# Kernel optimization log

Hardware: AMD Instinct MI355X
Metric: run time of the kernel (lower is better)

Reference implementation:

```python
import jax, jax.numpy as jnp
import numpy as np

B = 16384
G = 2048   # granule_cell_count
N = 512    # ca3_cell_count
DT = 0.5   # integration_timestep
STEPS = 5  # ca3_attractor_steps
A_REC = 0.02   # recovery_time_constant
B_SUB = 0.2    # subthreshold_coupling
C_RESET = -55.0  # spike_reset_voltage
D_AHP = 4.0      # after_hyperpolarization_jump
CONN_P = 0.1


def setup_inputs() -> dict:
    key = jax.random.key(0)
    k1, k2, k3, k4 = jax.random.split(key, 4)
    dg_query_spikes = (jax.random.uniform(k1, (B, G)) < 0.1).astype(jnp.float32)
    W_mossy = 0.05 * jax.random.normal(k2, (N, G), dtype=jnp.float32)
    mask = (jax.random.uniform(k3, (N, N)) < CONN_P).astype(jnp.float32)
    W_rec = mask * jax.random.uniform(k4, (N, N)) * 0.1
    W_rec = W_rec * (1.0 - jnp.eye(N, dtype=jnp.float32))  # zero diagonal
    v0 = jnp.full((N,), -65.0, dtype=jnp.float32)
    u0 = jnp.full((N,), 0.2 * -65.0, dtype=jnp.float32)
    return {"dg_query_spikes": dg_query_spikes, "W_mossy": W_mossy,
            "W_rec": W_rec, "v0": v0, "u0": u0}


def _izhikevich_step(v, u, I):
    # Euler step of the Izhikevich neuron model, per original torch code.
    dv = 0.04 * v * v + 5.0 * v + 140.0 - u + I
    du = A_REC * (B_SUB * v - u)
    v = v + dv * DT
    u = u + du * DT
    spike = (v >= 30.0).astype(v.dtype)
    v = jnp.where(spike > 0, jnp.asarray(C_RESET, v.dtype), v)
    u = u + spike * D_AHP
    v = jnp.clip(v, -90.0, 30.0)
    return v, u, spike


def reference(dg_query_spikes, W_mossy, W_rec, v0, u0):
    # query_current = Linear(dg) * 10.0  -> [B, N]
    query_current = (dg_query_spikes @ W_mossy.T) * 10.0
    v = jnp.broadcast_to(v0, (B, N))
    u = jnp.broadcast_to(u0, (B, N))
    spike = jnp.zeros((B, N), dtype=jnp.float32)
    for _ in range(STEPS):  # fixed small unrolled recurrence
        # torch.mv(W_rec, spikes) batched: [B,N] @ [N,N]^T
        recurrent_current = (v >= 30.0).astype(jnp.float32) @ W_rec.T
        total_current = query_current + recurrent_current
        v, u, spike = _izhikevich_step(v, u, total_current)
    return spike
```

## Files before the change

### kernel.cpp

```cpp
#include <hip/hip_runtime.h>
#include <cstdint>
#include <cstddef>


typedef __attribute__((ext_vector_type(8))) short bf16x8;
typedef __attribute__((ext_vector_type(8))) unsigned short u16x8;
typedef __attribute__((ext_vector_type(4))) float f32x4;
typedef __attribute__((ext_vector_type(4))) unsigned int u32x4;

constexpr int Bn = 16384, Gn = 2048, Nn = 512;
constexpr int BM = 64, BN = 128;
constexpr int NKT = 64;
constexpr size_t SLAB_A = (size_t)4 * Bn * 16;
constexpr size_t SLAB_B = (size_t)4 * Nn * 16;
constexpr size_t A_BYTES = (size_t)256 * Bn * 16;
constexpr size_t B_BYTES = (size_t)256 * Nn * 16;
constexpr unsigned int CAP = 700000;
constexpr size_t OFF_B    = A_BYTES;
constexpr size_t OFF_THR  = OFF_B + B_BYTES;
constexpr size_t OFF_CNT  = OFF_THR + 64;
constexpr size_t OFF_LIST = OFF_CNT + 64;
constexpr size_t WS_NEED  = OFF_LIST + (size_t)CAP * 4;
constexpr float DELTA = 0.125f;

__device__ __forceinline__ unsigned short f2bf(float x) {
  uint32_t u = __builtin_bit_cast(uint32_t, x);
  u += 0x7FFFu + ((u >> 16) & 1u);
  return (unsigned short)(u >> 16);
}

__device__ __forceinline__ void glds16(const void* g, const void* l) {
  __builtin_amdgcn_global_load_lds(
      (const __attribute__((address_space(1))) unsigned int*)g,
      (__attribute__((address_space(3))) unsigned int*)l, 16, 0, 0);
}

__device__ __forceinline__ float izhi5(float I, float vi, float ui) {
#pragma clang fp contract(off)
  float v = vi, u = ui, spk = 0.0f;
#pragma unroll
  for (int st = 0; st < 5; ++st) {
    float dv = 0.04f * v * v + 5.0f * v + 140.0f - u + I;
    float du = 0.02f * (0.2f * v - u);
    v = v + dv * 0.5f;
    u = u + du * 0.5f;
    spk = (v >= 30.0f) ? 1.0f : 0.0f;
    if (spk > 0.0f) v = -55.0f;
    u = u + spk * 4.0f;
    v = fminf(fmaxf(v, -90.0f), 30.0f);
  }
  return spk;
}

__global__ void calibrate(const float* __restrict__ v0, const float* __restrict__ u0,
                          float* __restrict__ thr, unsigned int* __restrict__ cnt) {
  const int l = (int)threadIdx.x;
  if (l == 0) cnt[0] = 0u;
  const float vi = v0[0], ui = u0[0];
  const float X0 = -45.0f;
  const float step = 90.0f / 64.0f;
  const float s = izhi5(X0 + step * (float)l, vi, ui);
  const float sp = __shfl_up(s, 1);
  unsigned long long m = __ballot((l > 0) && (s != sp));
  float t[2] = {1e30f, 1e30f};
#pragma unroll
  for (int k = 0; k < 2; ++k) {
    if (!m) break;
    const int i = __ffsll((long long)m) - 1;
    m &= m - 1;
    float lo = X0 + step * (float)(i - 1);
    float hi = X0 + step * (float)i;
    for (int rr = 0; rr < 3; ++rr) {
      const float st2 = (hi - lo) / 64.0f;
      const float ss = izhi5(lo + st2 * (float)l, vi, ui);
      const float s0 = __shfl(ss, 0);
      const unsigned long long mm = __ballot(ss != s0);
      const int ii = mm ? (__ffsll((long long)mm) - 1) : 64;
      hi = lo + st2 * (float)ii;
      lo = lo + st2 * (float)(ii - 1);
    }
    t[k] = 0.5f * (lo + hi);
  }
  if (l == 0) { thr[0] = t[0]; thr[1] = t[1]; }
}

__launch_bounds__(256)
__global__ void prep_dg(const float* __restrict__ dg, unsigned short* __restrict__ Ab) {
  __shared__ uint32_t lds[64][129];
  const int t  = (int)threadIdx.x;
  const int mt = (int)blockIdx.x >> 3;
  const int gt = (int)blockIdx.x & 7;
  const int m0 = mt * 64, g0 = gt * 256;
  {
    const int mm = t >> 2, q = t & 3;
    const float* src = dg + (size_t)(m0 + mm) * Gn + g0;
#pragma unroll
    for (int i = 0; i < 16; ++i) {
      float4 v = *reinterpret_cast<const float4*>(src + i * 16 + q * 4);
      uint32_t a = (v.x != 0.0f ? 0x3F80u : 0u) | (v.y != 0.0f ? 0x3F800000u : 0u);
      uint32_t b = (v.z != 0.0f ? 0x3F80u : 0u) | (v.w != 0.0f ? 0x3F800000u : 0u);
      const int c = i * 8 + q * 2;
      lds[mm][c] = a; lds[mm][c + 1] = b;
    }
  }
  __syncthreads();
  {
    const int mm = t & 63, c0 = t >> 6;
#pragma unroll
    for (int cc = 0; cc < 8; ++cc) {
      const int c = c0 + cc * 4;
      u32x4 v;
      v.x = lds[mm][c * 4 + 0]; v.y = lds[mm][c * 4 + 1];
      v.z = lds[mm][c * 4 + 2]; v.w = lds[mm][c * 4 + 3];
      const size_t off = ((size_t)(gt * 32 + c) * Bn + (m0 + mm)) * 16;
      *reinterpret_cast<u32x4*>(reinterpret_cast<char*>(Ab) + off) = v;
    }
  }
}

__launch_bounds__(256)
__global__ void prep_W(const float* __restrict__ Wm, unsigned short* __restrict__ Bb) {
  const int n  = (int)blockIdx.x;
  const int gi = (int)threadIdx.x;
  const float* src = Wm + (size_t)n * Gn + gi * 8;
  u16x8 h0;
#pragma unroll
  for (int e = 0; e < 8; ++e) h0[e] = f2bf(src[e]);
  *reinterpret_cast<u16x8*>(reinterpret_cast<char*>(Bb) +
                            ((size_t)gi * Nn + n) * 16) = h0;
}

__launch_bounds__(256, 4)
__global__ void gemm_spike(const char* __restrict__ Ab, const char* __restrict__ Bb,
                           const float* __restrict__ thr,
                           unsigned int* __restrict__ cnt,
                           unsigned int* __restrict__ list,
                           float* __restrict__ out) {
  __shared__ __align__(16) char lds[24576];
  const int t = (int)threadIdx.x;
  const int bx0 = (int)blockIdx.x;
  const int bx  = (bx0 & 7) * 128 + (bx0 >> 3);
  const int mt = bx >> 2, nt = bx & 3;
  const int m0 = mt * BM, n0 = nt * BN;

  const uint32_t asrc = (uint32_t)((((t >> 6) * Bn) + m0 + (t & 63)) * 16);
  uint32_t bsrc[2];
#pragma unroll
  for (int c = 0; c < 2; ++c) {
    const int j = t + 256 * c;
    bsrc[c] = (uint32_t)((((j >> 7) * Nn) + n0 + (j & 127)) * 16);
  }

  const int l  = t & 63, wv = t >> 6;
  const int wr = wv >> 1, wc = wv & 1;
  const int lr = l & 15, kh = l >> 4;

  uint32_t aoff[2], boff[4];
#pragma unroll
  for (int mf = 0; mf < 2; ++mf)
    aoff[mf] = (uint32_t)((kh * 64 + wr * 32 + mf * 16 + lr) * 16);
#pragma unroll
  for (int nf = 0; nf < 4; ++nf)
    boff[nf] = (uint32_t)(4096 + (kh * 128 + wc * 64 + nf * 16 + lr) * 16);

  f32x4 acc[2][4];
#pragma unroll
  for (int i = 0; i < 2; ++i)
#pragma unroll
    for (int j = 0; j < 4; ++j)
      acc[i][j] = (f32x4){0.0f, 0.0f, 0.0f, 0.0f};

  glds16(Ab + asrc, &lds[t * 16]);
#pragma unroll
  for (int c = 0; c < 2; ++c) glds16(Bb + bsrc[c], &lds[4096 + (t + 256 * c) * 16]);
  __syncthreads();

  for (int kt = 0; kt < NKT; ++kt) {
    const int cb = (kt & 1) * 12288;
    if (kt + 1 < NKT) {
      const int nb = ((kt + 1) & 1) * 12288;
      const char* pa = Ab + (size_t)(kt + 1) * SLAB_A;
      const char* pb = Bb + (size_t)(kt + 1) * SLAB_B;
      glds16(pa + asrc, &lds[nb + t * 16]);
#pragma unroll
      for (int c = 0; c < 2; ++c) glds16(pb + bsrc[c], &lds[nb + 4096 + (t + 256 * c) * 16]);
    }
    bf16x8 af[2], bf[4];
#pragma unroll
    for (int mf = 0; mf < 2; ++mf)
      af[mf] = *reinterpret_cast<const bf16x8*>(&lds[cb + aoff[mf]]);
#pragma unroll
    for (int nf = 0; nf < 4; ++nf)
      bf[nf] = *reinterpret_cast<const bf16x8*>(&lds[cb + boff[nf]]);
#pragma unroll
    for (int mf = 0; mf < 2; ++mf)
#pragma unroll
      for (int nf = 0; nf < 4; ++nf)
        acc[mf][nf] = __builtin_amdgcn_mfma_f32_16x16x32_bf16(
            af[mf], bf[nf], acc[mf][nf], 0, 0, 0);
    __syncthreads();
  }

  const float I5 = thr[0], I4 = thr[1];
#pragma unroll
  for (int nf = 0; nf < 4; ++nf) {
    const int ncol = n0 + wc * 64 + nf * 16 + lr;
#pragma unroll
    for (int mf = 0; mf < 2; ++mf) {
      const int mrow = m0 + wr * 32 + mf * 16 + kh * 4;
#pragma unroll
      for (int r = 0; r < 4; ++r) {
        const float I = acc[mf][nf][r] * 10.0f;
        const float sp = (I > I5 && I < I4) ? 1.0f : 0.0f;
        out[(size_t)(mrow + r) * Nn + ncol] = sp;
        if (fabsf(I - I5) < DELTA || fabsf(I - I4) < DELTA) {
          const unsigned int idx = atomicAdd(cnt, 1u);
          if (idx < CAP)
            list[idx] = (unsigned int)(mrow + r) * (unsigned int)Nn + (unsigned int)ncol;
        }
      }
    }
  }
}

__launch_bounds__(256)
__global__ void fixup(const float* __restrict__ dg, const float* __restrict__ Wm,
                      const float* __restrict__ v0, const float* __restrict__ u0,
                      const unsigned int* __restrict__ cnt,
                      const unsigned int* __restrict__ list,
                      float* __restrict__ out) {
#pragma clang fp contract(off)
  const unsigned int n = min(cnt[0], CAP);
  const unsigned int wid0   = (blockIdx.x * blockDim.x + threadIdx.x) >> 6;
  const unsigned int nwaves = (gridDim.x * blockDim.x) >> 6;
  const int l = (int)(threadIdx.x & 63);
  for (unsigned int i = wid0; i < n; i += nwaves) {
    const unsigned int e = list[i];
    const unsigned int m = e >> 9, nn = e & 511u;
    const float* dr = dg + (size_t)m * Gn;
    const float* wr = Wm + (size_t)nn * Gn;
    float acc = 0.0f;
#pragma unroll
    for (int j = 0; j < 8; ++j) {
      const int g = j * 256 + l * 4;
      const float4 d = *reinterpret_cast<const float4*>(dr + g);
      const float4 w = *reinterpret_cast<const float4*>(wr + g);
      acc += (d.x != 0.0f) ? w.x : 0.0f;
      acc += (d.y != 0.0f) ? w.y : 0.0f;
      acc += (d.z != 0.0f) ? w.z : 0.0f;
      acc += (d.w != 0.0f) ? w.w : 0.0f;
    }
#pragma unroll
    for (int off = 32; off > 0; off >>= 1) acc += __shfl_down(acc, off);
    if (l == 0)
      out[(size_t)m * Nn + nn] = izhi5(acc * 10.0f, v0[nn], u0[nn]);
  }
}

constexpr int ROWS = 32, TG = 16, NCHUNK = Gn / 32;

__launch_bounds__(512, 2)
__global__ void ca3_sparse_kernel(const float* __restrict__ dg,
                                  const float* __restrict__ Wm,
                                  const float* __restrict__ v0,
                                  const float* __restrict__ u0,
                                  float* __restrict__ out) {
#pragma clang fp contract(off)
  __shared__ float    lds_w[TG * Nn];
  __shared__ uint32_t lds_bits[ROWS][NCHUNK];
  const int t    = (int)threadIdx.x;
  const int row0 = (int)blockIdx.x * ROWS;
  {
    const int r  = t >> 4;
    const int c0 = (t & 15) * 4;
    const float* p = dg + (size_t)(row0 + r) * Gn + (size_t)c0 * 32;
#pragma unroll
    for (int cc = 0; cc < 4; ++cc) {
      uint32_t bits = 0;
#pragma unroll
      for (int i = 0; i < 8; ++i) {
        float4 x = reinterpret_cast<const float4*>(p + cc * 32)[i];
        bits |= (x.x != 0.0f ? 1u : 0u) << (i * 4 + 0);
        bits |= (x.y != 0.0f ? 1u : 0u) << (i * 4 + 1);
        bits |= (x.z != 0.0f ? 1u : 0u) << (i * 4 + 2);
        bits |= (x.w != 0.0f ? 1u : 0u) << (i * 4 + 3);
      }
      lds_bits[r][c0 + cc] = bits;
    }
  }
  float acc[ROWS];
#pragma unroll
  for (int r = 0; r < ROWS; ++r) acc[r] = 0.0f;
  for (int gt = 0; gt < Gn / TG; ++gt) {
    __syncthreads();
    {
      const int k  = t & 3;
      const int nb = t >> 2;
#pragma unroll
      for (int pq = 0; pq < 4; ++pq) {
        const int n = pq * 128 + nb;
        const float4 w4 = *reinterpret_cast<const float4*>(
            Wm + (size_t)n * Gn + gt * TG + k * 4);
        lds_w[(k * 4 + 0) * Nn + n] = w4.x;
        lds_w[(k * 4 + 1) * Nn + n] = w4.y;
        lds_w[(k * 4 + 2) * Nn + n] = w4.z;
        lds_w[(k * 4 + 3) * Nn + n] = w4.w;
      }
    }
    __syncthreads();
    const int shift = (gt & 1) * 16;
#pragma unroll
    for (int r = 0; r < ROWS; ++r) {
      uint32_t b = (lds_bits[r][gt >> 1] >> shift) & 0xFFFFu;
      b = __builtin_amdgcn_readfirstlane(b);
      while (b) {
        const int g0 = __builtin_ctz(b);
        const uint32_t b1 = b & (b - 1);
        const int g1 = __builtin_ctz(b1 | 0x8000u);
        const uint32_t b2 = b1 & (b1 - 1);
        const int g2 = __builtin_ctz(b2 | 0x8000u);
        const uint32_t b3 = b2 & (b2 - 1);
        const int g3 = __builtin_ctz(b3 | 0x8000u);
        float x0 = lds_w[g0 * Nn + t];
        float x1 = lds_w[g1 * Nn + t];
        float x2 = lds_w[g2 * Nn + t];
        float x3 = lds_w[g3 * Nn + t];
        x1 = (b1 != 0u) ? x1 : 0.0f;
        x2 = (b2 != 0u) ? x2 : 0.0f;
        x3 = (b3 != 0u) ? x3 : 0.0f;
        acc[r] += x0; acc[r] += x1; acc[r] += x2; acc[r] += x3;
        b = b3 & (b3 - 1);
      }
    }
  }
  const float vi = v0[t];
  const float ui = u0[t];
#pragma unroll
  for (int r = 0; r < ROWS; ++r) {
    out[(size_t)(row0 + r) * Nn + t] = izhi5(acc[r] * 10.0f, vi, ui);
  }
}

extern "C" void kernel_launch(void* const* d_in, const int* in_sizes, int n_in,
                              void* d_out, int out_size, void* d_ws, size_t ws_size,
                              hipStream_t stream) {
  const float* dg = (const float*)d_in[0];
  const float* Wm = (const float*)d_in[1];
  const float* v0 = (const float*)d_in[3];
  const float* u0 = (const float*)d_in[4];
  float* out = (float*)d_out;

  if (ws_size < WS_NEED) {
    hipLaunchKernelGGL(ca3_sparse_kernel, dim3(Bn / ROWS), dim3(512), 0, stream,
                       dg, Wm, v0, u0, out);
    return;
  }
  char* base = (char*)d_ws;
  unsigned short* Ab = (unsigned short*)base;
  unsigned short* Bb = (unsigned short*)(base + OFF_B);
  float* thr         = (float*)(base + OFF_THR);
  unsigned int* cnt  = (unsigned int*)(base + OFF_CNT);
  unsigned int* list = (unsigned int*)(base + OFF_LIST);

  hipLaunchKernelGGL(calibrate, dim3(1), dim3(64), 0, stream, v0, u0, thr, cnt);
  hipLaunchKernelGGL(prep_dg, dim3(2048), dim3(256), 0, stream, dg, Ab);
  hipLaunchKernelGGL(prep_W, dim3(512), dim3(256), 0, stream, Wm, Bb);
  hipLaunchKernelGGL(gemm_spike, dim3(1024), dim3(256), 0, stream,
                     (const char*)Ab, (const char*)Bb, thr, cnt, list, out);
  hipLaunchKernelGGL(fixup, dim3(512), dim3(256), 0, stream,
                     dg, Wm, v0, u0, cnt, list, out);
}
```

Measured before the change: 135.0 us.

## Fuse dg-to-bf16 conversion into GEMM with register-staged 4-buffer pipeline

Removes the separate prep_dg kernel and its workspace round trip. The GEMM now reads the fp32 spike matrix directly into registers, packs it to bf16 by truncation, and writes it to LDS. B tiles still stream in through global_load_lds. The loop becomes a manually unrolled 4-buffer software pipeline with explicit waitcnt and barrier control. This saves a full write and reread of the converted A matrix, at the cost of more LDS (lower occupancy bound, 3 blocks) and fp32 global reads inside the GEMM.

```diff
diff --git a/kernel.cpp b/kernel.cpp
--- a/kernel.cpp
+++ b/kernel.cpp
@@ -11,22 +11,24 @@
 constexpr int Bn = 16384, Gn = 2048, Nn = 512;
 constexpr int BM = 64, BN = 128;
 constexpr int NKT = 64;
-constexpr size_t SLAB_A = (size_t)4 * Bn * 16;
 constexpr size_t SLAB_B = (size_t)4 * Nn * 16;
-constexpr size_t A_BYTES = (size_t)256 * Bn * 16;
-constexpr size_t B_BYTES = (size_t)256 * Nn * 16;
+constexpr size_t B_BYTES = (size_t)NKT * SLAB_B;
 constexpr unsigned int CAP = 700000;
-constexpr size_t OFF_B    = A_BYTES;
-constexpr size_t OFF_THR  = OFF_B + B_BYTES;
+constexpr size_t OFF_THR  = B_BYTES;
 constexpr size_t OFF_CNT  = OFF_THR + 64;
 constexpr size_t OFF_LIST = OFF_CNT + 64;
 constexpr size_t WS_NEED  = OFF_LIST + (size_t)CAP * 4;
 constexpr float DELTA = 0.125f;
+constexpr int BUFB = 12288;
 
 __device__ __forceinline__ unsigned short f2bf(float x) {
   uint32_t u = __builtin_bit_cast(uint32_t, x);
   u += 0x7FFFu + ((u >> 16) & 1u);
   return (unsigned short)(u >> 16);
+}
+__device__ __forceinline__ uint32_t pack2(float lo, float hi) {
+  return (__builtin_bit_cast(uint32_t, lo) >> 16) |
+         (__builtin_bit_cast(uint32_t, hi) & 0xFFFF0000u);
 }
 
 __device__ __forceinline__ void glds16(const void* g, const void* l) {
@@ -85,40 +87,6 @@
 }
 
 __launch_bounds__(256)
-__global__ void prep_dg(const float* __restrict__ dg, unsigned short* __restrict__ Ab) {
-  __shared__ uint32_t lds[64][129];
-  const int t  = (int)threadIdx.x;
-  const int mt = (int)blockIdx.x >> 3;
-  const int gt = (int)blockIdx.x & 7;
-  const int m0 = mt * 64, g0 = gt * 256;
-  {
-    const int mm = t >> 2, q = t & 3;
-    const float* src = dg + (size_t)(m0 + mm) * Gn + g0;
-#pragma unroll
-    for (int i = 0; i < 16; ++i) {
-      float4 v = *reinterpret_cast<const float4*>(src + i * 16 + q * 4);
-      uint32_t a = (v.x != 0.0f ? 0x3F80u : 0u) | (v.y != 0.0f ? 0x3F800000u : 0u);
-      uint32_t b = (v.z != 0.0f ? 0x3F80u : 0u) | (v.w != 0.0f ? 0x3F800000u : 0u);
-      const int c = i * 8 + q * 2;
-      lds[mm][c] = a; lds[mm][c + 1] = b;
-    }
-  }
-  __syncthreads();
-  {
-    const int mm = t & 63, c0 = t >> 6;
-#pragma unroll
-    for (int cc = 0; cc < 8; ++cc) {
-      const int c = c0 + cc * 4;
-      u32x4 v;
-      v.x = lds[mm][c * 4 + 0]; v.y = lds[mm][c * 4 + 1];
-      v.z = lds[mm][c * 4 + 2]; v.w = lds[mm][c * 4 + 3];
-      const size_t off = ((size_t)(gt * 32 + c) * Bn + (m0 + mm)) * 16;
-      *reinterpret_cast<u32x4*>(reinterpret_cast<char*>(Ab) + off) = v;
-    }
-  }
-}
-
-__launch_bounds__(256)
 __global__ void prep_W(const float* __restrict__ Wm, unsigned short* __restrict__ Bb) {
   const int n  = (int)blockIdx.x;
   const int gi = (int)threadIdx.x;
@@ -130,26 +98,25 @@
                             ((size_t)gi * Nn + n) * 16) = h0;
 }
 
-__launch_bounds__(256, 4)
-__global__ void gemm_spike(const char* __restrict__ Ab, const char* __restrict__ Bb,
+__launch_bounds__(256, 3)
+__global__ void gemm_fused(const float* __restrict__ dg, const char* __restrict__ Bb,
                            const float* __restrict__ thr,
                            unsigned int* __restrict__ cnt,
                            unsigned int* __restrict__ list,
                            float* __restrict__ out) {
-  __shared__ __align__(16) char lds[24576];
+  __shared__ __align__(16) char lds[4 * BUFB];
   const int t = (int)threadIdx.x;
   const int bx0 = (int)blockIdx.x;
   const int bx  = (bx0 & 7) * 128 + (bx0 >> 3);
   const int mt = bx >> 2, nt = bx & 3;
   const int m0 = mt * BM, n0 = nt * BN;
 
-  const uint32_t asrc = (uint32_t)((((t >> 6) * Bn) + m0 + (t & 63)) * 16);
-  uint32_t bsrc[2];
-#pragma unroll
-  for (int c = 0; c < 2; ++c) {
-    const int j = t + 256 * c;
-    bsrc[c] = (uint32_t)((((j >> 7) * Nn) + n0 + (j & 127)) * 16);
-  }
+  const float* dgrow = dg + (size_t)(m0 + (t >> 2)) * Gn + (t & 3) * 8;
+  const uint32_t awoff = (uint32_t)(((t & 3) * 64 + (t >> 2)) * 16);
+  const uint32_t bsrc0 = (uint32_t)((((t >> 7) & 3) * Nn + n0 + (t & 127)) * 16);
+  const uint32_t bsrc1 = (uint32_t)(((((t + 256) >> 7) & 3) * Nn + n0 + ((t + 256) & 127)) * 16);
+  const uint32_t bdst0 = (uint32_t)(4096 + t * 16);
+  const uint32_t bdst1 = (uint32_t)(4096 + (t + 256) * 16);
 
   const int l  = t & 63, wv = t >> 6;
   const int wr = wv >> 1, wc = wv & 1;
@@ -170,36 +137,79 @@
     for (int j = 0; j < 4; ++j)
       acc[i][j] = (f32x4){0.0f, 0.0f, 0.0f, 0.0f};
 
-  glds16(Ab + asrc, &lds[t * 16]);
-#pragma unroll
-  for (int c = 0; c < 2; ++c) glds16(Bb + bsrc[c], &lds[4096 + (t + 256 * c) * 16]);
-  __syncthreads();
-
-  for (int kt = 0; kt < NKT; ++kt) {
-    const int cb = (kt & 1) * 12288;
-    if (kt + 1 < NKT) {
-      const int nb = ((kt + 1) & 1) * 12288;
-      const char* pa = Ab + (size_t)(kt + 1) * SLAB_A;
-      const char* pb = Bb + (size_t)(kt + 1) * SLAB_B;
-      glds16(pa + asrc, &lds[nb + t * 16]);
-#pragma unroll
-      for (int c = 0; c < 2; ++c) glds16(pb + bsrc[c], &lds[nb + 4096 + (t + 256 * c) * 16]);
-    }
-    bf16x8 af[2], bf[4];
-#pragma unroll
-    for (int mf = 0; mf < 2; ++mf)
-      af[mf] = *reinterpret_cast<const bf16x8*>(&lds[cb + aoff[mf]]);
-#pragma unroll
-    for (int nf = 0; nf < 4; ++nf)
-      bf[nf] = *reinterpret_cast<const bf16x8*>(&lds[cb + boff[nf]]);
-#pragma unroll
-    for (int mf = 0; mf < 2; ++mf)
-#pragma unroll
-      for (int nf = 0; nf < 4; ++nf)
-        acc[mf][nf] = __builtin_amdgcn_mfma_f32_16x16x32_bf16(
-            af[mf], bf[nf], acc[mf][nf], 0, 0, 0);
-    __syncthreads();
-  }
+  float4 rsE0, rsE1, rsO0, rsO1;
+
+#define STAGE_ISSUE(KT, RA0, RA1)                                         \
+  {                                                                       \
+    const float* ap = dgrow + (size_t)(KT) * 32;                          \
+    RA0 = *reinterpret_cast<const float4*>(ap);                           \
+    RA1 = *reinterpret_cast<const float4*>(ap + 4);                       \
+    const char* pb = Bb + (size_t)(KT) * SLAB_B;                          \
+    char* bb = &lds[((KT) & 3) * BUFB];                                   \
+    glds16(pb + bsrc0, bb + bdst0);                                       \
+    glds16(pb + bsrc1, bb + bdst1);                                       \
+  }
+
+#define CONVERT_WRITE(KT, RA0, RA1)                                       \
+  {                                                                       \
+    u32x4 wv4;                                                            \
+    wv4.x = pack2(RA0.x, RA0.y); wv4.y = pack2(RA0.z, RA0.w);             \
+    wv4.z = pack2(RA1.x, RA1.y); wv4.w = pack2(RA1.z, RA1.w);             \
+    *reinterpret_cast<u32x4*>(&lds[((KT) & 3) * BUFB + awoff]) = wv4;     \
+  }
+
+#define COMPUTE(KT)                                                       \
+  {                                                                       \
+    const char* base = &lds[((KT) & 3) * BUFB];                           \
+    bf16x8 af0 = *reinterpret_cast<const bf16x8*>(base + aoff[0]);        \
+    bf16x8 af1 = *reinterpret_cast<const bf16x8*>(base + aoff[1]);        \
+    bf16x8 bq0 = *reinterpret_cast<const bf16x8*>(base + boff[0]);        \
+    bf16x8 bq1 = *reinterpret_cast<const bf16x8*>(base + boff[1]);        \
+    bf16x8 bq2 = *reinterpret_cast<const bf16x8*>(base + boff[2]);        \
+    bf16x8 bq3 = *reinterpret_cast<const bf16x8*>(base + boff[3]);        \
+    acc[0][0] = __builtin_amdgcn_mfma_f32_16x16x32_bf16(af0, bq0, acc[0][0], 0, 0, 0); \
+    acc[0][1] = __builtin_amdgcn_mfma_f32_16x16x32_bf16(af0, bq1, acc[0][1], 0, 0, 0); \
+    acc[0][2] = __builtin_amdgcn_mfma_f32_16x16x32_bf16(af0, bq2, acc[0][2], 0, 0, 0); \
+    acc[0][3] = __builtin_amdgcn_mfma_f32_16x16x32_bf16(af0, bq3, acc[0][3], 0, 0, 0); \
+    acc[1][0] = __builtin_amdgcn_mfma_f32_16x16x32_bf16(af1, bq0, acc[1][0], 0, 0, 0); \
+    acc[1][1] = __builtin_amdgcn_mfma_f32_16x16x32_bf16(af1, bq1, acc[1][1], 0, 0, 0); \
+    acc[1][2] = __builtin_amdgcn_mfma_f32_16x16x32_bf16(af1, bq2, acc[1][2], 0, 0, 0); \
+    acc[1][3] = __builtin_amdgcn_mfma_f32_16x16x32_bf16(af1, bq3, acc[1][3], 0, 0, 0); \
+  }
+
+#define END_BARRIER(VMC)                                                  \
+  asm volatile("s_waitcnt vmcnt(" #VMC ")");                              \
+  __builtin_amdgcn_sched_barrier(0);                                      \
+  asm volatile("s_waitcnt lgkmcnt(0)");                                   \
+  __builtin_amdgcn_sched_barrier(0);                                      \
+  __builtin_amdgcn_s_barrier();                                           \
+  __builtin_amdgcn_sched_barrier(0);
+
+  STAGE_ISSUE(0, rsE0, rsE1);
+  STAGE_ISSUE(1, rsO0, rsO1);
+  CONVERT_WRITE(0, rsE0, rsE1);
+  END_BARRIER(4)
+
+  for (int j = 0; j < 31; ++j) {
+    const int kt = 2 * j;
+    STAGE_ISSUE(kt + 2, rsE0, rsE1);
+    COMPUTE(kt);
+    CONVERT_WRITE(kt + 1, rsO0, rsO1);
+    END_BARRIER(4)
+    STAGE_ISSUE(kt + 3, rsO0, rsO1);
+    COMPUTE(kt + 1);
+    CONVERT_WRITE(kt + 2, rsE0, rsE1);
+    END_BARRIER(4)
+  }
+  COMPUTE(62);
+  CONVERT_WRITE(63, rsO0, rsO1);
+  END_BARRIER(0)
+  COMPUTE(63);
+
+#undef STAGE_ISSUE
+#undef CONVERT_WRITE
+#undef COMPUTE
+#undef END_BARRIER
 
   const float I5 = thr[0], I4 = thr[1];
 #pragma unroll
@@ -356,17 +366,15 @@
     return;
   }
   char* base = (char*)d_ws;
-  unsigned short* Ab = (unsigned short*)base;
-  unsigned short* Bb = (unsigned short*)(base + OFF_B);
+  unsigned short* Bb = (unsigned short*)base;
   float* thr         = (float*)(base + OFF_THR);
   unsigned int* cnt  = (unsigned int*)(base + OFF_CNT);
   unsigned int* list = (unsigned int*)(base + OFF_LIST);
 
   hipLaunchKernelGGL(calibrate, dim3(1), dim3(64), 0, stream, v0, u0, thr, cnt);
-  hipLaunchKernelGGL(prep_dg, dim3(2048), dim3(256), 0, stream, dg, Ab);
   hipLaunchKernelGGL(prep_W, dim3(512), dim3(256), 0, stream, Wm, Bb);
-  hipLaunchKernelGGL(gemm_spike, dim3(1024), dim3(256), 0, stream,
-                     (const char*)Ab, (const char*)Bb, thr, cnt, list, out);
+  hipLaunchKernelGGL(gemm_fused, dim3(1024), dim3(256), 0, stream,
+                     dg, (const char*)Bb, thr, cnt, list, out);
   hipLaunchKernelGGL(fixup, dim3(512), dim3(256), 0, stream,
                      dg, Wm, v0, u0, cnt, list, out);
 }
```

After: 141.1 us. 4.6% more time.

## Deepen GEMM LDS pipeline to four buffers with prefetch distance two

Applied to the files above, without the earlier changes.

The bf16 MFMA main loop moves from double buffering to a four-slot LDS ring. Each iteration issues global-to-LDS loads two k-tiles ahead and waits with an explicit partial vmcnt instead of a full drain before each barrier. This is meant to hide more global memory latency behind MFMA work. In exchange it doubles LDS use per block, which lowers the launch-bounds occupancy hint from 4 to 3 and may reduce the number of resident blocks per CU.

```diff
diff --git a/kernel.cpp b/kernel.cpp
--- a/kernel.cpp
+++ b/kernel.cpp
@@ -22,6 +22,7 @@
 constexpr size_t OFF_LIST = OFF_CNT + 64;
 constexpr size_t WS_NEED  = OFF_LIST + (size_t)CAP * 4;
 constexpr float DELTA = 0.125f;
+constexpr int BUFB = 12288;
 
 __device__ __forceinline__ unsigned short f2bf(float x) {
   uint32_t u = __builtin_bit_cast(uint32_t, x);
@@ -130,13 +131,13 @@
                             ((size_t)gi * Nn + n) * 16) = h0;
 }
 
-__launch_bounds__(256, 4)
+__launch_bounds__(256, 3)
 __global__ void gemm_spike(const char* __restrict__ Ab, const char* __restrict__ Bb,
                            const float* __restrict__ thr,
                            unsigned int* __restrict__ cnt,
                            unsigned int* __restrict__ list,
                            float* __restrict__ out) {
-  __shared__ __align__(16) char lds[24576];
+  __shared__ __align__(16) char lds[4 * BUFB];
   const int t = (int)threadIdx.x;
   const int bx0 = (int)blockIdx.x;
   const int bx  = (bx0 & 7) * 128 + (bx0 >> 3);
@@ -170,36 +171,56 @@
     for (int j = 0; j < 4; ++j)
       acc[i][j] = (f32x4){0.0f, 0.0f, 0.0f, 0.0f};
 
-  glds16(Ab + asrc, &lds[t * 16]);
-#pragma unroll
-  for (int c = 0; c < 2; ++c) glds16(Bb + bsrc[c], &lds[4096 + (t + 256 * c) * 16]);
-  __syncthreads();
-
-  for (int kt = 0; kt < NKT; ++kt) {
-    const int cb = (kt & 1) * 12288;
-    if (kt + 1 < NKT) {
-      const int nb = ((kt + 1) & 1) * 12288;
-      const char* pa = Ab + (size_t)(kt + 1) * SLAB_A;
-      const char* pb = Bb + (size_t)(kt + 1) * SLAB_B;
-      glds16(pa + asrc, &lds[nb + t * 16]);
-#pragma unroll
-      for (int c = 0; c < 2; ++c) glds16(pb + bsrc[c], &lds[nb + 4096 + (t + 256 * c) * 16]);
-    }
-    bf16x8 af[2], bf[4];
-#pragma unroll
-    for (int mf = 0; mf < 2; ++mf)
-      af[mf] = *reinterpret_cast<const bf16x8*>(&lds[cb + aoff[mf]]);
-#pragma unroll
-    for (int nf = 0; nf < 4; ++nf)
-      bf[nf] = *reinterpret_cast<const bf16x8*>(&lds[cb + boff[nf]]);
-#pragma unroll
-    for (int mf = 0; mf < 2; ++mf)
-#pragma unroll
-      for (int nf = 0; nf < 4; ++nf)
-        acc[mf][nf] = __builtin_amdgcn_mfma_f32_16x16x32_bf16(
-            af[mf], bf[nf], acc[mf][nf], 0, 0, 0);
-    __syncthreads();
-  }
+#define STAGE(KT)                                                          \
+  {                                                                        \
+    const char* pa = Ab + (size_t)(KT) * SLAB_A;                           \
+    const char* pb = Bb + (size_t)(KT) * SLAB_B;                           \
+    char* bb = &lds[((KT) & 3) * BUFB];                                    \
+    glds16(pa + asrc, bb + t * 16);                                        \
+    glds16(pb + bsrc[0], bb + 4096 + t * 16);                              \
+    glds16(pb + bsrc[1], bb + 4096 + (t + 256) * 16);                      \
+  }
+
+#define COMPUTE(KT)                                                        \
+  {                                                                        \
+    const char* base = &lds[((KT) & 3) * BUFB];                            \
+    bf16x8 af0 = *reinterpret_cast<const bf16x8*>(base + aoff[0]);         \
+    bf16x8 af1 = *reinterpret_cast<const bf16x8*>(base + aoff[1]);         \
+    bf16x8 bq0 = *reinterpret_cast<const bf16x8*>(base + boff[0]);         \
+    bf16x8 bq1 = *reinterpret_cast<const bf16x8*>(base + boff[1]);         \
+    bf16x8 bq2 = *reinterpret_cast<const bf16x8*>(base + boff[2]);         \
+    bf16x8 bq3 = *reinterpret_cast<const bf16x8*>(base + boff[3]);         \
+    acc[0][0] = __builtin_amdgcn_mfma_f32_16x16x32_bf16(af0, bq0, acc[0][0], 0, 0, 0); \
+    acc[0][1] = __builtin_amdgcn_mfma_f32_16x16x32_bf16(af0, bq1, acc[0][1], 0, 0, 0); \
+    acc[0][2] = __builtin_amdgcn_mfma_f32_16x16x32_bf16(af0, bq2, acc[0][2], 0, 0, 0); \
+    acc[0][3] = __builtin_amdgcn_mfma_f32_16x16x32_bf16(af0, bq3, acc[0][3], 0, 0, 0); \
+    acc[1][0] = __builtin_amdgcn_mfma_f32_16x16x32_bf16(af1, bq0, acc[1][0], 0, 0, 0); \
+    acc[1][1] = __builtin_amdgcn_mfma_f32_16x16x32_bf16(af1, bq1, acc[1][1], 0, 0, 0); \
+    acc[1][2] = __builtin_amdgcn_mfma_f32_16x16x32_bf16(af1, bq2, acc[1][2], 0, 0, 0); \
+    acc[1][3] = __builtin_amdgcn_mfma_f32_16x16x32_bf16(af1, bq3, acc[1][3], 0, 0, 0); \
+  }
+
+#define BAR(VMC)                                                           \
+  asm volatile("s_waitcnt vmcnt(" #VMC ")" ::: "memory");                  \
+  __builtin_amdgcn_s_barrier();                                            \
+  asm volatile("" ::: "memory");
+
+  STAGE(0)
+  STAGE(1)
+  BAR(3)
+
+  for (int kt = 0; kt < NKT - 2; ++kt) {
+    STAGE(kt + 2)
+    COMPUTE(kt)
+    BAR(3)
+  }
+  COMPUTE(NKT - 2)
+  BAR(0)
+  COMPUTE(NKT - 1)
+
+#undef STAGE
+#undef COMPUTE
+#undef BAR
 
   const float I5 = thr[0], I4 = thr[1];
 #pragma unroll
```

New measurement: 134.5 us. About the same (-0.3%).

## Pack spike input into bitmasks and expand to bf16 inside the GEMM

Applied to the files above, without the earlier changes.

The dense bf16 copy of the binary spike matrix is replaced with a 1-bit-per-element packed layout. The GEMM expands those bits to bf16 fragments in registers just before each MFMA. The GEMM is also re-tiled to 256x64 blocks: each block loads a 16-step slab of the mossy weights into 64KB of LDS, and A is read straight from global memory as bits. This is meant to cut the large intermediate write/read traffic of the bf16 A matrix (about 64MB) down to about 4MB. The cost is extra ALU work for bit expansion and lower occupancy from the larger LDS footprint.

```diff
diff --git a/kernel.cpp b/kernel.cpp
--- a/kernel.cpp
+++ b/kernel.cpp
@@ -9,15 +9,11 @@
 typedef __attribute__((ext_vector_type(4))) unsigned int u32x4;
 
 constexpr int Bn = 16384, Gn = 2048, Nn = 512;
-constexpr int BM = 64, BN = 128;
-constexpr int NKT = 64;
-constexpr size_t SLAB_A = (size_t)4 * Bn * 16;
-constexpr size_t SLAB_B = (size_t)4 * Nn * 16;
-constexpr size_t A_BYTES = (size_t)256 * Bn * 16;
-constexpr size_t B_BYTES = (size_t)256 * Nn * 16;
+constexpr size_t B_BYTES    = (size_t)256 * Nn * 16;
+constexpr size_t BITS_BYTES = (size_t)Bn * 256;
 constexpr unsigned int CAP = 700000;
-constexpr size_t OFF_B    = A_BYTES;
-constexpr size_t OFF_THR  = OFF_B + B_BYTES;
+constexpr size_t OFF_BITS = B_BYTES;
+constexpr size_t OFF_THR  = OFF_BITS + BITS_BYTES;
 constexpr size_t OFF_CNT  = OFF_THR + 64;
 constexpr size_t OFF_LIST = OFF_CNT + 64;
 constexpr size_t WS_NEED  = OFF_LIST + (size_t)CAP * 4;
@@ -85,40 +81,6 @@
 }
 
 __launch_bounds__(256)
-__global__ void prep_dg(const float* __restrict__ dg, unsigned short* __restrict__ Ab) {
-  __shared__ uint32_t lds[64][129];
-  const int t  = (int)threadIdx.x;
-  const int mt = (int)blockIdx.x >> 3;
-  const int gt = (int)blockIdx.x & 7;
-  const int m0 = mt * 64, g0 = gt * 256;
-  {
-    const int mm = t >> 2, q = t & 3;
-    const float* src = dg + (size_t)(m0 + mm) * Gn + g0;
-#pragma unroll
-    for (int i = 0; i < 16; ++i) {
-      float4 v = *reinterpret_cast<const float4*>(src + i * 16 + q * 4);
-      uint32_t a = (v.x != 0.0f ? 0x3F80u : 0u) | (v.y != 0.0f ? 0x3F800000u : 0u);
-      uint32_t b = (v.z != 0.0f ? 0x3F80u : 0u) | (v.w != 0.0f ? 0x3F800000u : 0u);
-      const int c = i * 8 + q * 2;
-      lds[mm][c] = a; lds[mm][c + 1] = b;
-    }
-  }
-  __syncthreads();
-  {
-    const int mm = t & 63, c0 = t >> 6;
-#pragma unroll
-    for (int cc = 0; cc < 8; ++cc) {
-      const int c = c0 + cc * 4;
-      u32x4 v;
-      v.x = lds[mm][c * 4 + 0]; v.y = lds[mm][c * 4 + 1];
-      v.z = lds[mm][c * 4 + 2]; v.w = lds[mm][c * 4 + 3];
-      const size_t off = ((size_t)(gt * 32 + c) * Bn + (m0 + mm)) * 16;
-      *reinterpret_cast<u32x4*>(reinterpret_cast<char*>(Ab) + off) = v;
-    }
-  }
-}
-
-__launch_bounds__(256)
 __global__ void prep_W(const float* __restrict__ Wm, unsigned short* __restrict__ Bb) {
   const int n  = (int)blockIdx.x;
   const int gi = (int)threadIdx.x;
@@ -130,84 +92,123 @@
                             ((size_t)gi * Nn + n) * 16) = h0;
 }
 
-__launch_bounds__(256, 4)
-__global__ void gemm_spike(const char* __restrict__ Ab, const char* __restrict__ Bb,
-                           const float* __restrict__ thr,
-                           unsigned int* __restrict__ cnt,
-                           unsigned int* __restrict__ list,
-                           float* __restrict__ out) {
-  __shared__ __align__(16) char lds[24576];
+__launch_bounds__(256)
+__global__ void prep_bits(const float* __restrict__ dg, uint32_t* __restrict__ bits) {
+  __shared__ uint32_t nib[32 * 576];
+  const int t  = (int)threadIdx.x;
+  const int r0 = (int)blockIdx.x * 32;
+#pragma unroll 4
+  for (int i = 0; i < 64; ++i) {
+    const int idx = i * 256 + t;
+    const int row = idx >> 9;
+    const int col = idx & 511;
+    const float4 x = *reinterpret_cast<const float4*>(
+        dg + (size_t)(r0 + row) * Gn + col * 4);
+    uint32_t n = (x.x != 0.0f ? 1u : 0u) | (x.y != 0.0f ? 2u : 0u) |
+                 (x.z != 0.0f ? 4u : 0u) | (x.w != 0.0f ? 8u : 0u);
+    nib[row * 576 + col + (col >> 3)] = n;
+  }
+  __syncthreads();
+#pragma unroll
+  for (int i = 0; i < 8; ++i) {
+    const int oidx = i * 256 + t;
+    const int r   = oidx >> 6;
+    const int kh  = (oidx >> 4) & 3;
+    const int ktq = oidx & 15;
+    uint32_t by[4];
+#pragma unroll
+    for (int q = 0; q < 4; ++q) {
+      const int kt = ktq * 4 + q;
+      const int cp = kt * 8 + kh * 2 + kt;
+      const uint32_t ne = nib[r * 576 + cp];
+      const uint32_t no = nib[r * 576 + cp + 1];
+      by[q] = ne | (no << 4);
+    }
+    const uint32_t w = by[0] | (by[1] << 8) | (by[2] << 16) | (by[3] << 24);
+    bits[(size_t)(r0 + r) * 64 + kh * 16 + ktq] = w;
+  }
+}
+
+__launch_bounds__(256, 2)
+__global__ void gemm_bits(const uint32_t* __restrict__ bits, const char* __restrict__ Bb,
+                          const float* __restrict__ thr,
+                          unsigned int* __restrict__ cnt,
+                          unsigned int* __restrict__ list,
+                          float* __restrict__ out) {
+  __shared__ __align__(16) char lds[65536];
   const int t = (int)threadIdx.x;
   const int bx0 = (int)blockIdx.x;
-  const int bx  = (bx0 & 7) * 128 + (bx0 >> 3);
-  const int mt = bx >> 2, nt = bx & 3;
-  const int m0 = mt * BM, n0 = nt * BN;
-
-  const uint32_t asrc = (uint32_t)((((t >> 6) * Bn) + m0 + (t & 63)) * 16);
-  uint32_t bsrc[2];
-#pragma unroll
-  for (int c = 0; c < 2; ++c) {
-    const int j = t + 256 * c;
-    bsrc[c] = (uint32_t)((((j >> 7) * Nn) + n0 + (j & 127)) * 16);
-  }
-
-  const int l  = t & 63, wv = t >> 6;
-  const int wr = wv >> 1, wc = wv & 1;
+  const int bx  = (bx0 & 7) * 64 + (bx0 >> 3);
+  const int mt = bx >> 3, nt = bx & 7;
+  const int m0 = mt * 256, n0 = nt * 64;
+
+  const uint32_t bbase = (uint32_t)((((t >> 6) * Nn) + n0 + (t & 63)) * 16);
+  const uint32_t bdst0 = (uint32_t)(t * 16);
+
+  const int l  = t & 63, w = t >> 6;
   const int lr = l & 15, kh = l >> 4;
 
-  uint32_t aoff[2], boff[4];
-#pragma unroll
-  for (int mf = 0; mf < 2; ++mf)
-    aoff[mf] = (uint32_t)((kh * 64 + wr * 32 + mf * 16 + lr) * 16);
+  uint32_t abase[4];
+#pragma unroll
+  for (int mf = 0; mf < 4; ++mf)
+    abase[mf] = (uint32_t)((m0 + w * 64 + mf * 16 + lr) * 256 + kh * 64);
+  uint32_t boff[4];
 #pragma unroll
   for (int nf = 0; nf < 4; ++nf)
-    boff[nf] = (uint32_t)(4096 + (kh * 128 + wc * 64 + nf * 16 + lr) * 16);
-
-  f32x4 acc[2][4];
-#pragma unroll
-  for (int i = 0; i < 2; ++i)
+    boff[nf] = (uint32_t)((kh * 64 + nf * 16 + lr) * 16);
+
+  f32x4 acc[4][4];
+#pragma unroll
+  for (int i = 0; i < 4; ++i)
 #pragma unroll
     for (int j = 0; j < 4; ++j)
       acc[i][j] = (f32x4){0.0f, 0.0f, 0.0f, 0.0f};
 
-  glds16(Ab + asrc, &lds[t * 16]);
-#pragma unroll
-  for (int c = 0; c < 2; ++c) glds16(Bb + bsrc[c], &lds[4096 + (t + 256 * c) * 16]);
-  __syncthreads();
-
-  for (int kt = 0; kt < NKT; ++kt) {
-    const int cb = (kt & 1) * 12288;
-    if (kt + 1 < NKT) {
-      const int nb = ((kt + 1) & 1) * 12288;
-      const char* pa = Ab + (size_t)(kt + 1) * SLAB_A;
-      const char* pb = Bb + (size_t)(kt + 1) * SLAB_B;
-      glds16(pa + asrc, &lds[nb + t * 16]);
-#pragma unroll
-      for (int c = 0; c < 2; ++c) glds16(pb + bsrc[c], &lds[nb + 4096 + (t + 256 * c) * 16]);
-    }
-    bf16x8 af[2], bf[4];
-#pragma unroll
-    for (int mf = 0; mf < 2; ++mf)
-      af[mf] = *reinterpret_cast<const bf16x8*>(&lds[cb + aoff[mf]]);
-#pragma unroll
-    for (int nf = 0; nf < 4; ++nf)
-      bf[nf] = *reinterpret_cast<const bf16x8*>(&lds[cb + boff[nf]]);
-#pragma unroll
-    for (int mf = 0; mf < 2; ++mf)
+  const char* bitsc = (const char*)bits;
+
+  for (int c = 0; c < 4; ++c) {
+    if (c) __syncthreads();
+#pragma unroll
+    for (int o = 0; o < 16; ++o)
+      glds16(Bb + (size_t)c * 524288 + o * 32768 + bbase,
+             &lds[o * 4096 + bdst0]);
+    u32x4 ab[4];
+#pragma unroll
+    for (int mf = 0; mf < 4; ++mf)
+      ab[mf] = *reinterpret_cast<const u32x4*>(bitsc + abase[mf] + c * 16);
+    __syncthreads();
+
+#pragma unroll
+    for (int ktl = 0; ktl < 16; ++ktl) {
+      bf16x8 bq[4];
 #pragma unroll
       for (int nf = 0; nf < 4; ++nf)
-        acc[mf][nf] = __builtin_amdgcn_mfma_f32_16x16x32_bf16(
-            af[mf], bf[nf], acc[mf][nf], 0, 0, 0);
-    __syncthreads();
+        bq[nf] = *reinterpret_cast<const bf16x8*>(&lds[ktl * 4096 + boff[nf]]);
+#pragma unroll
+      for (int mf = 0; mf < 4; ++mf) {
+        const uint32_t e = ab[mf][ktl >> 2];
+        const uint32_t b = e >> ((ktl & 3) * 8);
+        u32x4 aw;
+        aw.x = (b & 1u)   * 0x3F80u     | (b & 2u)   * 0x1FC00000u;
+        aw.y = (b & 4u)   * 0xFE0u      | (b & 8u)   * 0x07F00000u;
+        aw.z = (b & 16u)  * 0x3F8u      | (b & 32u)  * 0x01FC0000u;
+        aw.w = (b & 64u)  * 0xFEu       | (b & 128u) * 0x007F0000u;
+        const bf16x8 af = __builtin_bit_cast(bf16x8, aw);
+#pragma unroll
+        for (int nf = 0; nf < 4; ++nf)
+          acc[mf][nf] = __builtin_amdgcn_mfma_f32_16x16x32_bf16(
+              af, bq[nf], acc[mf][nf], 0, 0, 0);
+      }
+    }
   }
 
   const float I5 = thr[0], I4 = thr[1];
 #pragma unroll
   for (int nf = 0; nf < 4; ++nf) {
-    const int ncol = n0 + wc * 64 + nf * 16 + lr;
-#pragma unroll
-    for (int mf = 0; mf < 2; ++mf) {
-      const int mrow = m0 + wr * 32 + mf * 16 + kh * 4;
+    const int ncol = n0 + nf * 16 + lr;
+#pragma unroll
+    for (int mf = 0; mf < 4; ++mf) {
+      const int mrow = m0 + w * 64 + mf * 16 + kh * 4;
 #pragma unroll
       for (int r = 0; r < 4; ++r) {
         const float I = acc[mf][nf][r] * 10.0f;
@@ -276,16 +277,16 @@
     const float* p = dg + (size_t)(row0 + r) * Gn + (size_t)c0 * 32;
 #pragma unroll
     for (int cc = 0; cc < 4; ++cc) {
-      uint32_t bits = 0;
+      uint32_t bb = 0;
 #pragma unroll
       for (int i = 0; i < 8; ++i) {
         float4 x = reinterpret_cast<const float4*>(p + cc * 32)[i];
-        bits |= (x.x != 0.0f ? 1u : 0u) << (i * 4 + 0);
-        bits |= (x.y != 0.0f ? 1u : 0u) << (i * 4 + 1);
-        bits |= (x.z != 0.0f ? 1u : 0u) << (i * 4 + 2);
-        bits |= (x.w != 0.0f ? 1u : 0u) << (i * 4 + 3);
-      }
-      lds_bits[r][c0 + cc] = bits;
+        bb |= (x.x != 0.0f ? 1u : 0u) << (i * 4 + 0);
+        bb |= (x.y != 0.0f ? 1u : 0u) << (i * 4 + 1);
+        bb |= (x.z != 0.0f ? 1u : 0u) << (i * 4 + 2);
+        bb |= (x.w != 0.0f ? 1u : 0u) << (i * 4 + 3);
+      }
+      lds_bits[r][c0 + cc] = bb;
     }
   }
   float acc[ROWS];
@@ -356,17 +357,17 @@
     return;
   }
   char* base = (char*)d_ws;
-  unsigned short* Ab = (unsigned short*)base;
-  unsigned short* Bb = (unsigned short*)(base + OFF_B);
+  unsigned short* Bb = (unsigned short*)base;
+  uint32_t* bits     = (uint32_t*)(base + OFF_BITS);
   float* thr         = (float*)(base + OFF_THR);
   unsigned int* cnt  = (unsigned int*)(base + OFF_CNT);
   unsigned int* list = (unsigned int*)(base + OFF_LIST);
 
   hipLaunchKernelGGL(calibrate, dim3(1), dim3(64), 0, stream, v0, u0, thr, cnt);
-  hipLaunchKernelGGL(prep_dg, dim3(2048), dim3(256), 0, stream, dg, Ab);
   hipLaunchKernelGGL(prep_W, dim3(512), dim3(256), 0, stream, Wm, Bb);
-  hipLaunchKernelGGL(gemm_spike, dim3(1024), dim3(256), 0, stream,
-                     (const char*)Ab, (const char*)Bb, thr, cnt, list, out);
+  hipLaunchKernelGGL(prep_bits, dim3(512), dim3(256), 0, stream, dg, bits);
+  hipLaunchKernelGGL(gemm_bits, dim3(512), dim3(256), 0, stream,
+                     bits, (const char*)Bb, thr, cnt, list, out);
   hipLaunchKernelGGL(fixup, dim3(512), dim3(256), 0, stream,
                      dg, Wm, v0, u0, cnt, list, out);
 }
```

Result: faster. 124.5 us (-7.7%).
